# Kernel tuning notes

Hardware: AMD Instinct MI355X
Metric: run time of the kernel (lower is better)

## Reference

```python
import jax, jax.numpy as jnp
import numpy as np

B, T, E, H, DK, FF = 8, 2048, 64, 8, 8, 256
EPS = 1e-5


def _ln(x, g, b):
    m = jnp.mean(x, axis=-1, keepdims=True)
    v = jnp.mean((x - m) ** 2, axis=-1, keepdims=True)
    return (x - m) * jax.lax.rsqrt(v + EPS) * g + b


def setup_inputs() -> dict:
    key = jax.random.key(0)
    ks = jax.random.split(key, 16)
    s = 0.05
    f32 = jnp.float32
    return {
        "x": jax.random.normal(ks[0], (B, T, E), f32),
        "Wq": jax.random.normal(ks[1], (E, E), f32) * s,
        "bq": jnp.zeros((E,), f32),
        "Wk": jax.random.normal(ks[2], (E, E), f32) * s,
        "bk": jnp.zeros((E,), f32),
        "Wv": jax.random.normal(ks[3], (E, E), f32) * s,
        "bv": jnp.zeros((E,), f32),
        "Wo": jax.random.normal(ks[4], (E, E), f32) * s,
        "bo": jnp.zeros((E,), f32),
        "theta_attn": jax.random.uniform(ks[5], (), f32, 0.0, 2.0 * np.pi),
        "theta_ffn": jax.random.uniform(ks[6], (), f32, 0.0, 2.0 * np.pi),
        "W1": jax.random.normal(ks[7], (FF, E), f32) * s,
        "b1": jnp.zeros((FF,), f32),
        "W2": jax.random.normal(ks[8], (E, FF), f32) * s,
        "b2": jnp.zeros((E,), f32),
        "g1": jnp.ones((E,), f32),
        "be1": jnp.zeros((E,), f32),
        "g2": jnp.ones((E,), f32),
        "be2": jnp.zeros((E,), f32),
    }


def _forward(x, Wq, bq, Wk, bk, Wv, bv, Wo, bo, theta_attn, theta_ffn,
             W1, b1, W2, b2, g1, be1, g2, be2):
    def split(h):  # [B,T,E] -> [B,H,T,DK]
        return h.reshape(B, T, H, DK).transpose(0, 2, 1, 3)

    q = split(x @ Wq.T + bq)
    k = split(x @ Wk.T + bk)
    v = split(x @ Wv.T + bv)
    # per-head quantum circuit: RX(x) then shared RX(theta) -> <Z> = cos(x + theta)
    q = jnp.cos(q + theta_attn)
    k = jnp.cos(k + theta_attn)
    v = jnp.cos(v + theta_attn)
    scores = jnp.einsum('bhtd,bhsd->bhts', q, k) / np.float32(np.sqrt(DK))
    scores = jax.nn.softmax(scores, axis=-1)
    attn = jnp.einsum('bhts,bhsd->bhtd', scores, v)
    attn = attn.transpose(0, 2, 1, 3).reshape(B, T, E) @ Wo.T + bo
    x1 = _ln(x + attn, g1, be1)
    # FFN quantum circuit: RX(x) then shared RY(theta) -> <Z> = cos(x)*cos(theta)
    qout = jnp.cos(x1) * jnp.cos(theta_ffn)
    f = jax.nn.relu(qout @ W1.T + b1) @ W2.T + b2
    return _ln(x1 + f, g2, be2)


def reference(x, Wq, bq, Wk, bk, Wv, bv, Wo, bo, theta_attn, theta_ffn,
              W1, b1, W2, b2, g1, be1, g2, be2):
    return _forward(x, Wq, bq, Wk, bk, Wv, bv, Wo, bo, theta_attn, theta_ffn,
                    W1, b1, W2, b2, g1, be1, g2, be2)
```

## Files before the change

### kernel.cpp

```cpp
#include <hip/hip_runtime.h>
#include <hip/hip_bf16.h>

#define B_ 8
#define T_ 2048
#define NROWS 16384

typedef __attribute__((ext_vector_type(16))) float f32x16;
typedef __attribute__((ext_vector_type(8))) short short8;
typedef __fp16 half2_t __attribute__((ext_vector_type(2)));
typedef __fp16 half8_t __attribute__((ext_vector_type(8)));

__device__ __forceinline__ unsigned int pkrtz(float a, float b) {
    half2_t h = __builtin_amdgcn_cvt_pkrtz(a, b);
    return __builtin_bit_cast(unsigned int, h);
}
__device__ __forceinline__ unsigned int pkbf(float a, float b) {
    return __builtin_amdgcn_perm(__float_as_uint(b), __float_as_uint(a), 0x07060302u);
}
__device__ __forceinline__ float dot2(unsigned int a, unsigned int b, float c) {
    return __builtin_amdgcn_fdot2(__builtin_bit_cast(half2_t, a),
                                  __builtin_bit_cast(half2_t, b), c, false);
}
__device__ __forceinline__ float fast_exp2(float x) {
#if __has_builtin(__builtin_amdgcn_exp2f)
    return __builtin_amdgcn_exp2f(x);
#else
    return exp2f(x);
#endif
}

__global__ __launch_bounds__(512, 2) void qkv_kernel(
    const float* __restrict__ x,
    const float* __restrict__ Wq, const float* __restrict__ bq,
    const float* __restrict__ Wk, const float* __restrict__ bk,
    const float* __restrict__ Wv, const float* __restrict__ bv,
    const float* __restrict__ theta_attn,
    unsigned short* __restrict__ qb, unsigned short* __restrict__ kbuf,
    unsigned short* __restrict__ vbuf)
{
    __shared__ unsigned int xpk[32 * 66];
    __shared__ unsigned int wpk[32 * 196];
    __shared__ unsigned int outs[6144];
    const int tid = threadIdx.x;
    const int n0 = blockIdx.x * 64;

    #pragma unroll
    for (int t = 0; t < 2; t++) {
        int fi = tid + t * 512;
        float4 v = ((const float4*)(x + (size_t)n0 * 64))[fi];
        int r = fi >> 4, k0 = (fi & 15) * 4;
        xpk[(k0 >> 1) * 66 + r] = pkrtz(v.x, v.y);
        xpk[((k0 >> 1) + 1) * 66 + r] = pkrtz(v.z, v.w);
    }
    const float* Wm[3] = {Wq, Wk, Wv};
    #pragma unroll
    for (int t = 0; t < 6; t++) {
        int fi = tid + t * 512;
        int m = fi >> 10, j = (fi >> 4) & 63, k0 = (fi & 15) * 4;
        float4 v = ((const float4*)Wm[m])[fi & 1023];
        wpk[(k0 >> 1) * 196 + m * 64 + j] = pkrtz(v.x, v.y);
        wpk[((k0 >> 1) + 1) * 196 + m * 64 + j] = pkrtz(v.z, v.w);
    }
    __syncthreads();

    const int r0 = (tid & 31) * 2;
    const int c0 = (tid >> 5) * 12;
    float acc[2][12] = {};
    #pragma unroll 8
    for (int kp = 0; kp < 32; kp++) {
        uint2 a = *(const uint2*)&xpk[kp * 66 + r0];
        uint4 b0 = *(const uint4*)&wpk[kp * 196 + c0];
        uint4 b1 = *(const uint4*)&wpk[kp * 196 + c0 + 4];
        uint4 b2 = *(const uint4*)&wpk[kp * 196 + c0 + 8];
        unsigned int bb[12] = {b0.x, b0.y, b0.z, b0.w,
                               b1.x, b1.y, b1.z, b1.w,
                               b2.x, b2.y, b2.z, b2.w};
        #pragma unroll
        for (int j = 0; j < 12; j++) {
            acc[0][j] = dot2(a.x, bb[j], acc[0][j]);
            acc[1][j] = dot2(a.y, bb[j], acc[1][j]);
        }
    }

    {
        const float th = *theta_attn;
        const float QS = 0.51006980f;
        const float* biasp[3] = {bq, bk, bv};
        float bcol[12];
        #pragma unroll
        for (int j = 0; j < 12; j++) {
            int c = c0 + j;
            bcol[j] = biasp[c >> 6][c & 63];
        }
        #pragma unroll
        for (int i = 0; i < 2; i++) {
            float vals[12];
            #pragma unroll
            for (int j = 0; j < 12; j++) {
                float v = __cosf(acc[i][j] + bcol[j] + th);
                vals[j] = ((c0 + j) >> 6) == 0 ? v * QS : v;
            }
            int row = r0 + i;
            #pragma unroll
            for (int t = 0; t < 6; t++) {
                int c = c0 + 2 * t;
                outs[(c >> 3) * 256 + row * 4 + ((c & 7) >> 1)] = pkbf(vals[2*t], vals[2*t+1]);
            }
        }
    }
    __syncthreads();

    unsigned short* outp3[3] = {qb, kbuf, vbuf};
    #pragma unroll
    for (int t = 0; t < 3; t++) {
        int fi = tid + t * 512;
        int bh = fi >> 6, r2 = fi & 63;
        int m = bh >> 3, hI = bh & 7;
        uint4 v = *(const uint4*)&outs[4 * fi];
        int n = n0 + r2;
        unsigned short* dst = outp3[m] +
            ((size_t)((n >> 11) * 8 + hI) * 2048 + (n & 2047)) * 8;
        *(uint4*)dst = v;
    }
}

__global__ __launch_bounds__(256, 2) void attn_kernel(
    const unsigned short* __restrict__ qb,
    const unsigned short* __restrict__ kbuf,
    const unsigned short* __restrict__ vbuf,
    float* __restrict__ attn)
{
    __shared__ __align__(16) unsigned short Ks[1024 * 8];
    __shared__ __align__(16) unsigned short Vt[9 * 1032];
    const int tid = threadIdx.x;
    const int head = blockIdx.x >> 3;
    const int qseg = blockIdx.x & 7;
    const size_t hoff = (size_t)head * T_ * 8;
    const int wave = tid >> 6, lane = tid & 63;
    const int col = lane & 31, h = lane >> 5;
    const int q0 = qseg * 256 + wave * 64;

    const short8 z8 = {0, 0, 0, 0, 0, 0, 0, 0};
    short8 bqf0 = z8, bqf1 = z8;
    if (h == 0) {
        bqf0 = *(const short8*)(qb + hoff + (size_t)(q0 + col) * 8);
        bqf1 = *(const short8*)(qb + hoff + (size_t)(q0 + 32 + col) * 8);
    }

    if (tid < 128)
        ((uint4*)(Vt + 8 * 1032))[tid] =
            make_uint4(0x3f803f80u, 0x3f803f80u, 0x3f803f80u, 0x3f803f80u);

    f32x16 oacc0 = {0.f,0.f,0.f,0.f,0.f,0.f,0.f,0.f,0.f,0.f,0.f,0.f,0.f,0.f,0.f,0.f};
    f32x16 oacc1 = oacc0;
    const f32x16 z16 = oacc0;
    const unsigned short* vbase = &Vt[(col < 9 ? col : 8) * 1032 + 8 * h];
    short8 ak = z8;

    for (int half = 0; half < 2; half++) {
        __syncthreads();
        {
            const uint4* kg = (const uint4*)(kbuf + hoff + (size_t)half * 1024 * 8);
            const uint4* vg = (const uint4*)(vbuf + hoff + (size_t)half * 1024 * 8);
            #pragma unroll
            for (int it = 0; it < 4; it++) {
                int s = tid + it * 256;
                ((uint4*)Ks)[s] = kg[s];
                union { uint4 u; unsigned short us[8]; } cv;
                cv.u = vg[s];
                int sp = (s & ~12) | ((s & 4) << 1) | ((s & 8) >> 1);
                #pragma unroll
                for (int d = 0; d < 8; d++) Vt[d * 1032 + sp] = cv.us[d];
            }
        }
        __syncthreads();

        for (int s0 = 0; s0 < 1024; s0 += 32) {
            if (h == 0) ak = *(const short8*)&Ks[(s0 + col) * 8];
            short8 av0 = *(const short8*)&vbase[s0];
            short8 av1 = *(const short8*)&vbase[s0 + 16];

            f32x16 S0 = __builtin_amdgcn_mfma_f32_32x32x16_bf16(ak, bqf0, z16, 0, 0, 0);
            {
                union { unsigned int u[4]; short8 s; } bp;
                bp.u[0] = pkbf(fast_exp2(S0[0]), fast_exp2(S0[1]));
                bp.u[1] = pkbf(fast_exp2(S0[2]), fast_exp2(S0[3]));
                bp.u[2] = pkbf(fast_exp2(S0[4]), fast_exp2(S0[5]));
                bp.u[3] = pkbf(fast_exp2(S0[6]), fast_exp2(S0[7]));
                oacc0 = __builtin_amdgcn_mfma_f32_32x32x16_bf16(av0, bp.s, oacc0, 0, 0, 0);
                bp.u[0] = pkbf(fast_exp2(S0[8]),  fast_exp2(S0[9]));
                bp.u[1] = pkbf(fast_exp2(S0[10]), fast_exp2(S0[11]));
                bp.u[2] = pkbf(fast_exp2(S0[12]), fast_exp2(S0[13]));
                bp.u[3] = pkbf(fast_exp2(S0[14]), fast_exp2(S0[15]));
                oacc0 = __builtin_amdgcn_mfma_f32_32x32x16_bf16(av1, bp.s, oacc0, 0, 0, 0);
            }
            f32x16 S1 = __builtin_amdgcn_mfma_f32_32x32x16_bf16(ak, bqf1, z16, 0, 0, 0);
            {
                union { unsigned int u[4]; short8 s; } bp;
                bp.u[0] = pkbf(fast_exp2(S1[0]), fast_exp2(S1[1]));
                bp.u[1] = pkbf(fast_exp2(S1[2]), fast_exp2(S1[3]));
                bp.u[2] = pkbf(fast_exp2(S1[4]), fast_exp2(S1[5]));
                bp.u[3] = pkbf(fast_exp2(S1[6]), fast_exp2(S1[7]));
                oacc1 = __builtin_amdgcn_mfma_f32_32x32x16_bf16(av0, bp.s, oacc1, 0, 0, 0);
                bp.u[0] = pkbf(fast_exp2(S1[8]),  fast_exp2(S1[9]));
                bp.u[1] = pkbf(fast_exp2(S1[10]), fast_exp2(S1[11]));
                bp.u[2] = pkbf(fast_exp2(S1[12]), fast_exp2(S1[13]));
                bp.u[3] = pkbf(fast_exp2(S1[14]), fast_exp2(S1[15]));
                oacc1 = __builtin_amdgcn_mfma_f32_32x32x16_bf16(av1, bp.s, oacc1, 0, 0, 0);
            }
        }
    }

    const int bI = head >> 3, hI = head & 7;
    {
        float tot = oacc0[4];
        tot += __shfl_xor(tot, 32);
        const float inv = 1.0f / tot;
        const int q = q0 + col;
        #pragma unroll
        for (int rr = 0; rr < 4; rr++) {
            int d = 4 * h + rr;
            attn[((size_t)bI * 2048 + q) * 64 + hI * 8 + d] = oacc0[rr] * inv;
        }
    }
    {
        float tot = oacc1[4];
        tot += __shfl_xor(tot, 32);
        const float inv = 1.0f / tot;
        const int q = q0 + 32 + col;
        #pragma unroll
        for (int rr = 0; rr < 4; rr++) {
            int d = 4 * h + rr;
            attn[((size_t)bI * 2048 + q) * 64 + hI * 8 + d] = oacc1[rr] * inv;
        }
    }
}

__global__ __launch_bounds__(512, 4) void tail_kernel(
    const float* __restrict__ attn, const float* __restrict__ x,
    const float* __restrict__ Wo, const float* __restrict__ bo,
    const float* __restrict__ g1, const float* __restrict__ be1,
    const float* __restrict__ theta_ffn,
    const float* __restrict__ W1, const float* __restrict__ b1,
    const float* __restrict__ W2, const float* __restrict__ b2,
    const float* __restrict__ g2, const float* __restrict__ be2,
    float* __restrict__ outp)
{
    __shared__ unsigned int smem[15744];
    const int tid = threadIdx.x;
    const int lane = tid & 63;
    const int wave = tid >> 6;
    const int h = lane >> 5;
    const int n0 = blockIdx.x * 32;
    const int mrow = tid >> 4;
    const int c0 = (tid & 15) * 4;

    unsigned int* const W1p = smem;
    unsigned int* const W2p = smem;
    unsigned int* const Atp = smem + 9216;
    unsigned int* const qoutp = smem + 9216;
    unsigned int* const Wop = smem + 10368;
    unsigned int* const hrowp = smem + 10368;
    float* const Yf = (float*)(smem + 12672);
    float* const Y2a = (float*)(smem + 14592);
    float* const Y2b = (float*)(smem + 8448);

    const f32x16 z16 = {0.f,0.f,0.f,0.f,0.f,0.f,0.f,0.f,0.f,0.f,0.f,0.f,0.f,0.f,0.f,0.f};

    float4 atv = ((const float4*)(attn + (size_t)n0 * 64))[tid];
    float4 wo0 = ((const float4*)Wo)[tid];
    float4 wo1 = ((const float4*)Wo)[tid + 512];
    float4 xv = *(const float4*)(x + (size_t)(n0 + mrow) * 64 + c0);
    float4 w1r[8];
    #pragma unroll
    for (int t = 0; t < 8; t++) w1r[t] = ((const float4*)W1)[tid + t * 512];

    {
        int r = tid >> 4, k0 = (tid & 15) * 4;
        uint2 a2 = make_uint2(pkrtz(atv.x, atv.y), pkrtz(atv.z, atv.w));
        *(uint2*)&Atp[r * 36 + (k0 >> 1)] = a2;
        uint2 wa = make_uint2(pkrtz(wo0.x, wo0.y), pkrtz(wo0.z, wo0.w));
        *(uint2*)&Wop[r * 36 + (k0 >> 1)] = wa;
        int fi = tid + 512;
        int e1 = fi >> 4, k1 = (fi & 15) * 4;
        uint2 wb = make_uint2(pkrtz(wo1.x, wo1.y), pkrtz(wo1.z, wo1.w));
        *(uint2*)&Wop[e1 * 36 + (k1 >> 1)] = wb;
    }
    __syncthreads();

    #pragma unroll
    for (int t = 0; t < 8; t++) {
        int fi = tid + t * 512;
        int f = fi >> 4, k0 = (fi & 15) * 4;
        uint2 w2 = make_uint2(pkrtz(w1r[t].x, w1r[t].y), pkrtz(w1r[t].z, w1r[t].w));
        *(uint2*)&W1p[f * 36 + (k0 >> 1)] = w2;
    }

    if (wave < 2) {
        const int colo = wave * 32 + (lane & 31);
        f32x16 acc = z16;
        #pragma unroll
        for (int kk = 0; kk < 4; kk++) {
            half8_t a = __builtin_bit_cast(half8_t,
                *(const uint4*)&Atp[(lane & 31) * 36 + kk * 8 + h * 4]);
            half8_t b = __builtin_bit_cast(half8_t,
                *(const uint4*)&Wop[colo * 36 + kk * 8 + h * 4]);
            acc = __builtin_amdgcn_mfma_f32_32x32x16_f16(a, b, acc, 0, 0, 0);
        }
        float bov = bo[colo];
        #pragma unroll
        for (int reg = 0; reg < 16; reg++) {
            int rr = (reg & 3) + 8 * (reg >> 2) + 4 * h;
            Yf[rr * 68 + colo] = acc[reg] + bov;
        }
    }
    __syncthreads();

    float x1v[4];
    {
        float4 yv = *(const float4*)&Yf[mrow * 68 + c0];
        float vv[4] = {xv.x + yv.x, xv.y + yv.y, xv.z + yv.z, xv.w + yv.w};
        float s1 = vv[0] + vv[1] + vv[2] + vv[3];
        float s2 = vv[0]*vv[0] + vv[1]*vv[1] + vv[2]*vv[2] + vv[3]*vv[3];
        #pragma unroll
        for (int m = 1; m <= 8; m <<= 1) {
            s1 += __shfl_xor(s1, m);
            s2 += __shfl_xor(s2, m);
        }
        float mean = s1 * 0.015625f;
        float rstd = rsqrtf(s2 * 0.015625f - mean * mean + 1e-5f);
        float4 g14 = *(const float4*)&g1[c0];
        float4 be14 = *(const float4*)&be1[c0];
        float gg[4] = {g14.x, g14.y, g14.z, g14.w};
        float eb[4] = {be14.x, be14.y, be14.z, be14.w};
        float cth = __cosf(*theta_ffn);
        float qv[4];
        #pragma unroll
        for (int j = 0; j < 4; j++) {
            x1v[j] = (vv[j] - mean) * rstd * gg[j] + eb[j];
            qv[j] = __cosf(x1v[j]) * cth;
        }
        uint2 q2 = make_uint2(pkrtz(qv[0], qv[1]), pkrtz(qv[2], qv[3]));
        *(uint2*)&qoutp[mrow * 36 + (c0 >> 1)] = q2;
    }
    __syncthreads();

    float4 w2r[8];
    #pragma unroll
    for (int t = 0; t < 8; t++) w2r[t] = ((const float4*)W2)[tid + t * 512];

    {
        const int fl = lane & 31;
        f32x16 acc = z16;
        #pragma unroll
        for (int kk = 0; kk < 4; kk++) {
            half8_t a = __builtin_bit_cast(half8_t,
                *(const uint4*)&W1p[(wave * 32 + fl) * 36 + kk * 8 + h * 4]);
            half8_t b = __builtin_bit_cast(half8_t,
                *(const uint4*)&qoutp[fl * 36 + kk * 8 + h * 4]);
            acc = __builtin_amdgcn_mfma_f32_32x32x16_f16(a, b, acc, 0, 0, 0);
        }
        const int row = lane & 31;
        #pragma unroll
        for (int q = 0; q < 4; q++) {
            int fb = wave * 32 + 8 * q + 4 * h;
            float4 b1v = *(const float4*)&b1[fb];
            float h0 = fmaxf(acc[4*q+0] + b1v.x, 0.f);
            float h1 = fmaxf(acc[4*q+1] + b1v.y, 0.f);
            float h2 = fmaxf(acc[4*q+2] + b1v.z, 0.f);
            float h3 = fmaxf(acc[4*q+3] + b1v.w, 0.f);
            uint2 hp = make_uint2(pkrtz(h0, h1), pkrtz(h2, h3));
            *(uint2*)&hrowp[row * 132 + (fb >> 1)] = hp;
        }
    }
    __syncthreads();

    #pragma unroll
    for (int t = 0; t < 8; t++) {
        int fi = tid + t * 512;
        int e = fi >> 6, k0 = (fi & 63) * 4;
        uint2 w2 = make_uint2(pkrtz(w2r[t].x, w2r[t].y), pkrtz(w2r[t].z, w2r[t].w));
        *(uint2*)&W2p[e * 132 + (k0 >> 1)] = w2;
    }
    __syncthreads();

    if (wave < 2) {
        const int colo = wave * 32 + (lane & 31);
        f32x16 acc = z16;
        #pragma unroll
        for (int kk = 0; kk < 16; kk++) {
            half8_t a = __builtin_bit_cast(half8_t,
                *(const uint4*)&hrowp[(lane & 31) * 132 + kk * 8 + h * 4]);
            half8_t b = __builtin_bit_cast(half8_t,
                *(const uint4*)&W2p[colo * 132 + kk * 8 + h * 4]);
            acc = __builtin_amdgcn_mfma_f32_32x32x16_f16(a, b, acc, 0, 0, 0);
        }
        float b2v = b2[colo];
        float* Ydst = wave ? Y2b : Y2a;
        const int cl = lane & 31;
        #pragma unroll
        for (int reg = 0; reg < 16; reg++) {
            int rr = (reg & 3) + 8 * (reg >> 2) + 4 * h;
            Ydst[rr * 36 + cl] = acc[reg] + b2v;
        }
    }
    __syncthreads();

    {
        float4 fv = (c0 < 32) ? *(const float4*)&Y2a[mrow * 36 + c0]
                              : *(const float4*)&Y2b[mrow * 36 + (c0 - 32)];
        float vv[4] = {x1v[0] + fv.x, x1v[1] + fv.y, x1v[2] + fv.z, x1v[3] + fv.w};
        float s1 = vv[0] + vv[1] + vv[2] + vv[3];
        float s2 = vv[0]*vv[0] + vv[1]*vv[1] + vv[2]*vv[2] + vv[3]*vv[3];
        #pragma unroll
        for (int m = 1; m <= 8; m <<= 1) {
            s1 += __shfl_xor(s1, m);
            s2 += __shfl_xor(s2, m);
        }
        float mean = s1 * 0.015625f;
        float rstd = rsqrtf(s2 * 0.015625f - mean * mean + 1e-5f);
        float4 g24 = *(const float4*)&g2[c0];
        float4 be24 = *(const float4*)&be2[c0];
        float4 o;
        o.x = (vv[0] - mean) * rstd * g24.x + be24.x;
        o.y = (vv[1] - mean) * rstd * g24.y + be24.y;
        o.z = (vv[2] - mean) * rstd * g24.z + be24.z;
        o.w = (vv[3] - mean) * rstd * g24.w + be24.w;
        *(float4*)(outp + (size_t)(n0 + mrow) * 64 + c0) = o;
    }
}

extern "C" void kernel_launch(void* const* d_in, const int* in_sizes, int n_in,
                              void* d_out, int out_size, void* d_ws, size_t ws_size,
                              hipStream_t stream)
{
    const float* x   = (const float*)d_in[0];
    const float* Wq  = (const float*)d_in[1];
    const float* bq  = (const float*)d_in[2];
    const float* Wk  = (const float*)d_in[3];
    const float* bk  = (const float*)d_in[4];
    const float* Wv  = (const float*)d_in[5];
    const float* bv  = (const float*)d_in[6];
    const float* Wo  = (const float*)d_in[7];
    const float* bo  = (const float*)d_in[8];
    const float* tha = (const float*)d_in[9];
    const float* thf = (const float*)d_in[10];
    const float* W1  = (const float*)d_in[11];
    const float* b1  = (const float*)d_in[12];
    const float* W2  = (const float*)d_in[13];
    const float* b2  = (const float*)d_in[14];
    const float* g1  = (const float*)d_in[15];
    const float* be1 = (const float*)d_in[16];
    const float* g2  = (const float*)d_in[17];
    const float* be2 = (const float*)d_in[18];

    char* wsb = (char*)d_ws;
    unsigned short* qbp = (unsigned short*)(wsb);
    unsigned short* kbp = (unsigned short*)(wsb + (2u << 20));
    unsigned short* vbp = (unsigned short*)(wsb + (4u << 20));
    float* attn = (float*)(wsb + (6u << 20));

    qkv_kernel<<<256, 512, 0, stream>>>(x, Wq, bq, Wk, bk, Wv, bv, tha, qbp, kbp, vbp);
    attn_kernel<<<512, 256, 0, stream>>>(qbp, kbp, vbp, attn);
    tail_kernel<<<512, 512, 0, stream>>>(attn, x, Wo, bo, g1, be1, thf,
                                         W1, b1, W2, b2, g2, be2, (float*)d_out);
}
```

Baseline: 140.1 us.

## Pre-transpose V in QKV kernel and split attention keys across wave halves

The QKV kernel now writes V directly in the transposed, permuted layout the attention MFMA expects, so the attention kernel no longer stages K and V through shared memory. Attention blocks grow to 512 threads, with two wave groups each handling half of the key range and their partial accumulators and row sums merged through a small LDS buffer. This removes the LDS transpose and the per-half barriers and doubles the number of waves in flight. The cost is direct global or cache reads of K and V inside the inner loop, plus an extra reduction step.

```diff
diff --git a/kernel.cpp b/kernel.cpp
--- a/kernel.cpp
+++ b/kernel.cpp
@@ -36,7 +36,7 @@
     const float* __restrict__ Wv, const float* __restrict__ bv,
     const float* __restrict__ theta_attn,
     unsigned short* __restrict__ qb, unsigned short* __restrict__ kbuf,
-    unsigned short* __restrict__ vbuf)
+    unsigned short* __restrict__ vt)
 {
     __shared__ unsigned int xpk[32 * 66];
     __shared__ unsigned int wpk[32 * 196];
@@ -110,128 +110,152 @@
     }
     __syncthreads();
 
-    unsigned short* outp3[3] = {qb, kbuf, vbuf};
-    #pragma unroll
-    for (int t = 0; t < 3; t++) {
+    unsigned short* outp2[2] = {qb, kbuf};
+    #pragma unroll
+    for (int t = 0; t < 2; t++) {
         int fi = tid + t * 512;
         int bh = fi >> 6, r2 = fi & 63;
         int m = bh >> 3, hI = bh & 7;
         uint4 v = *(const uint4*)&outs[4 * fi];
         int n = n0 + r2;
-        unsigned short* dst = outp3[m] +
+        unsigned short* dst = outp2[m] +
             ((size_t)((n >> 11) * 8 + hI) * 2048 + (n & 2047)) * 8;
         *(uint4*)dst = v;
     }
-}
-
-__global__ __launch_bounds__(256, 2) void attn_kernel(
+    {
+        int head = tid >> 6, d = (tid >> 3) & 7, j = tid & 7;
+        int bh = 16 + head, dw = d >> 1, hb = d & 1;
+        const unsigned short* ob = (const unsigned short*)outs;
+        union { uint4 u; unsigned short us[8]; } pk;
+        #pragma unroll
+        for (int e = 0; e < 8; e++) {
+            int sp = 8 * j + e;
+            int r = (sp & ~12) | ((sp & 4) << 1) | ((sp & 8) >> 1);
+            pk.us[e] = ob[(bh * 256 + r * 4 + dw) * 2 + hb];
+        }
+        int bI = n0 >> 11, tI0 = n0 & 2047;
+        int half = tI0 >> 10, s0v = tI0 & 1023;
+        size_t idx = ((((size_t)(bI * 8 + head) * 2 + half) * 8 + d) * 1024 + s0v + 8 * j);
+        *(uint4*)(vt + idx) = pk.u;
+    }
+}
+
+__global__ __launch_bounds__(512, 4) void attn_kernel(
     const unsigned short* __restrict__ qb,
     const unsigned short* __restrict__ kbuf,
-    const unsigned short* __restrict__ vbuf,
+    const unsigned short* __restrict__ vt,
     float* __restrict__ attn)
 {
-    __shared__ __align__(16) unsigned short Ks[1024 * 8];
-    __shared__ __align__(16) unsigned short Vt[9 * 1032];
+    __shared__ float comb[4][2][64][5];
     const int tid = threadIdx.x;
     const int head = blockIdx.x >> 3;
     const int qseg = blockIdx.x & 7;
     const size_t hoff = (size_t)head * T_ * 8;
     const int wave = tid >> 6, lane = tid & 63;
+    const int t = wave & 3, kh = wave >> 2;
     const int col = lane & 31, h = lane >> 5;
-    const int q0 = qseg * 256 + wave * 64;
+    const int q0 = qseg * 256 + t * 64;
 
     const short8 z8 = {0, 0, 0, 0, 0, 0, 0, 0};
+    union { uint4 u; short8 s; } onesu;
+    onesu.u = make_uint4(0x3f803f80u, 0x3f803f80u, 0x3f803f80u, 0x3f803f80u);
+
     short8 bqf0 = z8, bqf1 = z8;
     if (h == 0) {
         bqf0 = *(const short8*)(qb + hoff + (size_t)(q0 + col) * 8);
         bqf1 = *(const short8*)(qb + hoff + (size_t)(q0 + 32 + col) * 8);
     }
 
-    if (tid < 128)
-        ((uint4*)(Vt + 8 * 1032))[tid] =
-            make_uint4(0x3f803f80u, 0x3f803f80u, 0x3f803f80u, 0x3f803f80u);
-
     f32x16 oacc0 = {0.f,0.f,0.f,0.f,0.f,0.f,0.f,0.f,0.f,0.f,0.f,0.f,0.f,0.f,0.f,0.f};
     f32x16 oacc1 = oacc0;
     const f32x16 z16 = oacc0;
-    const unsigned short* vbase = &Vt[(col < 9 ? col : 8) * 1032 + 8 * h];
+
+    const unsigned short* krow = kbuf + hoff + (size_t)kh * 1024 * 8;
+    const unsigned short* vrow =
+        vt + (((size_t)head * 2 + kh) * 8 + (col < 8 ? col : 0)) * 1024 + 8 * h;
+
     short8 ak = z8;
-
-    for (int half = 0; half < 2; half++) {
-        __syncthreads();
+    short8 av0 = onesu.s, av1 = onesu.s;
+
+    #pragma unroll 2
+    for (int s0 = 0; s0 < 1024; s0 += 32) {
+        if (h == 0) ak = *(const short8*)&krow[(s0 + col) * 8];
+        if (col < 8) {
+            av0 = *(const short8*)&vrow[s0];
+            av1 = *(const short8*)&vrow[s0 + 16];
+        }
+        f32x16 S0 = __builtin_amdgcn_mfma_f32_32x32x16_bf16(ak, bqf0, z16, 0, 0, 0);
+        f32x16 S1 = __builtin_amdgcn_mfma_f32_32x32x16_bf16(ak, bqf1, z16, 0, 0, 0);
         {
-            const uint4* kg = (const uint4*)(kbuf + hoff + (size_t)half * 1024 * 8);
-            const uint4* vg = (const uint4*)(vbuf + hoff + (size_t)half * 1024 * 8);
+            union { unsigned int u[4]; short8 s; } bp;
+            bp.u[0] = pkbf(fast_exp2(S0[0]), fast_exp2(S0[1]));
+            bp.u[1] = pkbf(fast_exp2(S0[2]), fast_exp2(S0[3]));
+            bp.u[2] = pkbf(fast_exp2(S0[4]), fast_exp2(S0[5]));
+            bp.u[3] = pkbf(fast_exp2(S0[6]), fast_exp2(S0[7]));
+            oacc0 = __builtin_amdgcn_mfma_f32_32x32x16_bf16(av0, bp.s, oacc0, 0, 0, 0);
+            bp.u[0] = pkbf(fast_exp2(S0[8]),  fast_exp2(S0[9]));
+            bp.u[1] = pkbf(fast_exp2(S0[10]), fast_exp2(S0[11]));
+            bp.u[2] = pkbf(fast_exp2(S0[12]), fast_exp2(S0[13]));
+            bp.u[3] = pkbf(fast_exp2(S0[14]), fast_exp2(S0[15]));
+            oacc0 = __builtin_amdgcn_mfma_f32_32x32x16_bf16(av1, bp.s, oacc0, 0, 0, 0);
+        }
+        {
+            union { unsigned int u[4]; short8 s; } bp;
+            bp.u[0] = pkbf(fast_exp2(S1[0]), fast_exp2(S1[1]));
+            bp.u[1] = pkbf(fast_exp2(S1[2]), fast_exp2(S1[3]));
+            bp.u[2] = pkbf(fast_exp2(S1[4]), fast_exp2(S1[5]));
+            bp.u[3] = pkbf(fast_exp2(S1[6]), fast_exp2(S1[7]));
+            oacc1 = __builtin_amdgcn_mfma_f32_32x32x16_bf16(av0, bp.s, oacc1, 0, 0, 0);
+            bp.u[0] = pkbf(fast_exp2(S1[8]),  fast_exp2(S1[9]));
+            bp.u[1] = pkbf(fast_exp2(S1[10]), fast_exp2(S1[11]));
+            bp.u[2] = pkbf(fast_exp2(S1[12]), fast_exp2(S1[13]));
+            bp.u[3] = pkbf(fast_exp2(S1[14]), fast_exp2(S1[15]));
+            oacc1 = __builtin_amdgcn_mfma_f32_32x32x16_bf16(av1, bp.s, oacc1, 0, 0, 0);
+        }
+    }
+
+    __syncthreads();
+    if (kh == 1) {
+        #pragma unroll
+        for (int r = 0; r < 4; r++) {
+            comb[t][0][lane][r] = oacc0[r];
+            comb[t][1][lane][r] = oacc1[r];
+        }
+        comb[t][0][lane][4] = oacc0[4];
+        comb[t][1][lane][4] = oacc1[4];
+    }
+    __syncthreads();
+    if (kh == 0) {
+        #pragma unroll
+        for (int r = 0; r < 4; r++) {
+            oacc0[r] += comb[t][0][lane][r];
+            oacc1[r] += comb[t][1][lane][r];
+        }
+        oacc0[4] += comb[t][0][lane][4];
+        oacc1[4] += comb[t][1][lane][4];
+
+        const int bI = head >> 3, hI = head & 7;
+        {
+            float tot = oacc0[4];
+            tot += __shfl_xor(tot, 32);
+            const float inv = 2.0f / tot;
+            const int q = q0 + col;
             #pragma unroll
-            for (int it = 0; it < 4; it++) {
-                int s = tid + it * 256;
-                ((uint4*)Ks)[s] = kg[s];
-                union { uint4 u; unsigned short us[8]; } cv;
-                cv.u = vg[s];
-                int sp = (s & ~12) | ((s & 4) << 1) | ((s & 8) >> 1);
-                #pragma unroll
-                for (int d = 0; d < 8; d++) Vt[d * 1032 + sp] = cv.us[d];
+            for (int rr = 0; rr < 4; rr++) {
+                int d = 4 * h + rr;
+                attn[((size_t)bI * 2048 + q) * 64 + hI * 8 + d] = oacc0[rr] * inv;
             }
         }
-        __syncthreads();
-
-        for (int s0 = 0; s0 < 1024; s0 += 32) {
-            if (h == 0) ak = *(const short8*)&Ks[(s0 + col) * 8];
-            short8 av0 = *(const short8*)&vbase[s0];
-            short8 av1 = *(const short8*)&vbase[s0 + 16];
-
-            f32x16 S0 = __builtin_amdgcn_mfma_f32_32x32x16_bf16(ak, bqf0, z16, 0, 0, 0);
-            {
-                union { unsigned int u[4]; short8 s; } bp;
-                bp.u[0] = pkbf(fast_exp2(S0[0]), fast_exp2(S0[1]));
-                bp.u[1] = pkbf(fast_exp2(S0[2]), fast_exp2(S0[3]));
-                bp.u[2] = pkbf(fast_exp2(S0[4]), fast_exp2(S0[5]));
-                bp.u[3] = pkbf(fast_exp2(S0[6]), fast_exp2(S0[7]));
-                oacc0 = __builtin_amdgcn_mfma_f32_32x32x16_bf16(av0, bp.s, oacc0, 0, 0, 0);
-                bp.u[0] = pkbf(fast_exp2(S0[8]),  fast_exp2(S0[9]));
-                bp.u[1] = pkbf(fast_exp2(S0[10]), fast_exp2(S0[11]));
-                bp.u[2] = pkbf(fast_exp2(S0[12]), fast_exp2(S0[13]));
-                bp.u[3] = pkbf(fast_exp2(S0[14]), fast_exp2(S0[15]));
-                oacc0 = __builtin_amdgcn_mfma_f32_32x32x16_bf16(av1, bp.s, oacc0, 0, 0, 0);
+        {
+            float tot = oacc1[4];
+            tot += __shfl_xor(tot, 32);
+            const float inv = 2.0f / tot;
+            const int q = q0 + 32 + col;
+            #pragma unroll
+            for (int rr = 0; rr < 4; rr++) {
+                int d = 4 * h + rr;
+                attn[((size_t)bI * 2048 + q) * 64 + hI * 8 + d] = oacc1[rr] * inv;
             }
-            f32x16 S1 = __builtin_amdgcn_mfma_f32_32x32x16_bf16(ak, bqf1, z16, 0, 0, 0);
-            {
-                union { unsigned int u[4]; short8 s; } bp;
-                bp.u[0] = pkbf(fast_exp2(S1[0]), fast_exp2(S1[1]));
-                bp.u[1] = pkbf(fast_exp2(S1[2]), fast_exp2(S1[3]));
-                bp.u[2] = pkbf(fast_exp2(S1[4]), fast_exp2(S1[5]));
-                bp.u[3] = pkbf(fast_exp2(S1[6]), fast_exp2(S1[7]));
-                oacc1 = __builtin_amdgcn_mfma_f32_32x32x16_bf16(av0, bp.s, oacc1, 0, 0, 0);
-                bp.u[0] = pkbf(fast_exp2(S1[8]),  fast_exp2(S1[9]));
-                bp.u[1] = pkbf(fast_exp2(S1[10]), fast_exp2(S1[11]));
-                bp.u[2] = pkbf(fast_exp2(S1[12]), fast_exp2(S1[13]));
-                bp.u[3] = pkbf(fast_exp2(S1[14]), fast_exp2(S1[15]));
-                oacc1 = __builtin_amdgcn_mfma_f32_32x32x16_bf16(av1, bp.s, oacc1, 0, 0, 0);
-            }
-        }
-    }
-
-    const int bI = head >> 3, hI = head & 7;
-    {
-        float tot = oacc0[4];
-        tot += __shfl_xor(tot, 32);
-        const float inv = 1.0f / tot;
-        const int q = q0 + col;
-        #pragma unroll
-        for (int rr = 0; rr < 4; rr++) {
-            int d = 4 * h + rr;
-            attn[((size_t)bI * 2048 + q) * 64 + hI * 8 + d] = oacc0[rr] * inv;
-        }
-    }
-    {
-        float tot = oacc1[4];
-        tot += __shfl_xor(tot, 32);
-        const float inv = 1.0f / tot;
-        const int q = q0 + 32 + col;
-        #pragma unroll
-        for (int rr = 0; rr < 4; rr++) {
-            int d = 4 * h + rr;
-            attn[((size_t)bI * 2048 + q) * 64 + hI * 8 + d] = oacc1[rr] * inv;
         }
     }
 }
@@ -457,11 +481,11 @@
     char* wsb = (char*)d_ws;
     unsigned short* qbp = (unsigned short*)(wsb);
     unsigned short* kbp = (unsigned short*)(wsb + (2u << 20));
-    unsigned short* vbp = (unsigned short*)(wsb + (4u << 20));
+    unsigned short* vtp = (unsigned short*)(wsb + (4u << 20));
     float* attn = (float*)(wsb + (6u << 20));
 
-    qkv_kernel<<<256, 512, 0, stream>>>(x, Wq, bq, Wk, bk, Wv, bv, tha, qbp, kbp, vbp);
-    attn_kernel<<<512, 256, 0, stream>>>(qbp, kbp, vbp, attn);
+    qkv_kernel<<<256, 512, 0, stream>>>(x, Wq, bq, Wk, bk, Wv, bv, tha, qbp, kbp, vtp);
+    attn_kernel<<<512, 512, 0, stream>>>(qbp, kbp, vtp, attn);
     tail_kernel<<<512, 512, 0, stream>>>(attn, x, Wo, bo, g1, be1, thf,
                                          W1, b1, W2, b2, g2, be2, (float*)d_out);
 }
```

Measured after the change: 141.4 us. Within noise of the previous version (+0.9%).
